# Performance work log

Measured on AMD Instinct MI355X. Metric: run time of the kernel, lower is better.

## Reference

```python
import jax, jax.numpy as jnp
import numpy as np

EPS = 1e-8  # torch F.cosine_similarity eps
TEMP = 2.0  # hardcoded in module regardless of init arg


def _normalize(x):
    # row-normalize with torch-style eps clamp on the norm
    norm = jnp.sqrt(jnp.sum(x * x, axis=-1, keepdims=True))
    return x / jnp.maximum(norm, EPS)


def setup_inputs() -> dict:
    key = jax.random.key(0)
    k1, k2, k3 = jax.random.split(key, 3)
    n, m, d = 8192, 8192, 256
    return {
        "pos_key": jax.random.normal(k1, (n, d), dtype=jnp.float32),
        "pos_value": jax.random.normal(k2, (n, d), dtype=jnp.float32),
        "neg_value": jax.random.normal(k3, (m, d), dtype=jnp.float32),
    }


def reference(pos_key, pos_value, neg_value):
    pk = _normalize(pos_key)    # [n, d]
    pv = _normalize(pos_value)  # [n, d]
    nv = _normalize(neg_value)  # [m, d]

    pos_sim = jnp.sum(pk * pv, axis=-1)          # [n]
    neg_sim = jnp.einsum("nd,md->nm", pk, nv)    # [n, m] cosine sims

    pos_loss = -jnp.mean(pos_sim / TEMP)
    # log-sum-exp over m (stable), matching log(sum(exp(.)))
    neg_loss = jnp.mean(jax.scipy.special.logsumexp(neg_sim / TEMP, axis=-1))
    return pos_loss + neg_loss
```

## Files before the change

### kernel.cpp

```cpp
#include <hip/hip_runtime.h>

typedef __attribute__((ext_vector_type(4))) float f32x4;
typedef __attribute__((ext_vector_type(4))) int   i32x4;
typedef __attribute__((ext_vector_type(8))) int   i32x8;

#define DIM 256
#define D4  64

#define GLD_LDS16(g, l) __builtin_amdgcn_global_load_lds(                      \
    (const __attribute__((address_space(1))) void*)(g),                        \
    (__attribute__((address_space(3))) void*)(l), 16, 0, 0)

__global__ __launch_bounds__(256) void normalize_kernel(
    const float4* __restrict__ pk, const float4* __restrict__ pv,
    const float4* __restrict__ nv, unsigned int* __restrict__ pkn,
    unsigned int* __restrict__ nvn, float* __restrict__ posPart, int N) {
  int row  = blockIdx.x * 4 + (threadIdx.x >> 6);
  int lane = threadIdx.x & 63;
  if (row < N) {
    float4 x = pk[row * D4 + lane];
    float4 y = pv[row * D4 + lane];
    float skk = x.x*x.x + x.y*x.y + x.z*x.z + x.w*x.w;
    float svv = y.x*y.x + y.y*y.y + y.z*y.z + y.w*y.w;
    float skv = x.x*y.x + x.y*y.y + x.z*y.z + x.w*y.w;
#pragma unroll
    for (int m = 32; m >= 1; m >>= 1) {
      skk += __shfl_xor(skk, m, 64);
      svv += __shfl_xor(svv, m, 64);
      skv += __shfl_xor(skv, m, 64);
    }
    float nk  = fmaxf(sqrtf(skk), 1e-8f);
    float nvv = fmaxf(sqrtf(svv), 1e-8f);
    if (lane == 0) posPart[row] = skv / (nk * nvv);
    float rk = 1.0f / nk;
    int w = __builtin_amdgcn_cvt_pk_fp8_f32(x.x * rk, x.y * rk, 0, false);
    w = __builtin_amdgcn_cvt_pk_fp8_f32(x.z * rk, x.w * rk, w, true);
    pkn[(size_t)row * 64 + lane] = (unsigned int)w;
  } else {
    int r2 = row - N;
    float4 x = nv[r2 * D4 + lane];
    float s = x.x*x.x + x.y*x.y + x.z*x.z + x.w*x.w;
#pragma unroll
    for (int m = 32; m >= 1; m >>= 1) s += __shfl_xor(s, m, 64);
    float rn = 1.0f / fmaxf(sqrtf(s), 1e-8f);
    int w = __builtin_amdgcn_cvt_pk_fp8_f32(x.x * rn, x.y * rn, 0, false);
    w = __builtin_amdgcn_cvt_pk_fp8_f32(x.z * rn, x.w * rn, w, true);
    nvn[(size_t)r2 * 64 + lane] = (unsigned int)w;
  }
}

__global__ __launch_bounds__(256, 2) void gemm_lse_kernel(
    const unsigned char* __restrict__ gA, const unsigned char* __restrict__ gB,
    float* __restrict__ partial, int N) {
  __shared__ unsigned char Bs[2][32768];

  const int tid  = threadIdx.x;
  const int lane = tid & 63;
  const int wv   = tid >> 6;
  const int wm   = wv >> 1, wn = wv & 1;
  const int l15  = lane & 15, q = lane >> 4;
  const int row0 = blockIdx.y * 128;
  const int ct0  = blockIdx.x * 8;
  const float kLog2eHalf = 0.72134752044448170f;
  const int kUnitScale = 0x7F7F7F7F;

  const unsigned char* pa = gA + (size_t)(row0 + wm * 64 + l15) * 256 + q * 32;
  i32x4 alo[2][4], ahi[2][4];
#pragma unroll
  for (int kb = 0; kb < 2; kb++)
#pragma unroll
    for (int mi = 0; mi < 4; mi++) {
      alo[kb][mi] = *(const i32x4*)(pa + mi * 4096 + kb * 128);
      ahi[kb][mi] = *(const i32x4*)(pa + mi * 4096 + kb * 128 + 16);
    }

  {
    const unsigned char* pb = gB + (size_t)(ct0 * 128) * 256;
#pragma unroll
    for (int i = 0; i < 8; i++) {
      int c  = i * 256 + tid;
      int r  = c >> 4;
      int sc = ((c & 15) ^ (r & 15)) << 4;
      GLD_LDS16(pb + (size_t)r * 256 + sc, &Bs[0][c * 16]);
    }
  }
  __syncthreads();

  for (int ct = 0; ct < 8; ct++) {
    if (ct < 7) {
      const unsigned char* pb = gB + (size_t)((ct0 + ct + 1) * 128) * 256;
      unsigned char* dst = Bs[(ct + 1) & 1];
#pragma unroll
      for (int i = 0; i < 8; i++) {
        int c  = i * 256 + tid;
        int r  = c >> 4;
        int sc = ((c & 15) ^ (r & 15)) << 4;
        GLD_LDS16(pb + (size_t)r * 256 + sc, dst + c * 16);
      }
    }

    const unsigned char* bs = Bs[ct & 1];
    f32x4 acc[4][4];
#pragma unroll
    for (int mi = 0; mi < 4; mi++)
#pragma unroll
      for (int ni = 0; ni < 4; ni++) acc[mi][ni] = (f32x4){0.f, 0.f, 0.f, 0.f};

#pragma unroll
    for (int kb = 0; kb < 2; kb++) {
      i32x8 bf[4];
#pragma unroll
      for (int ni = 0; ni < 4; ni++) {
        int r  = wn * 64 + ni * 16 + l15;
        int c0 = (kb * 8 + q * 2)     ^ (r & 15);
        int c1 = (kb * 8 + q * 2 + 1) ^ (r & 15);
        i32x4 lo = *(const i32x4*)(bs + r * 256 + c0 * 16);
        i32x4 hi = *(const i32x4*)(bs + r * 256 + c1 * 16);
        bf[ni] = (i32x8){lo.x, lo.y, lo.z, lo.w, hi.x, hi.y, hi.z, hi.w};
      }
#pragma unroll
      for (int mi = 0; mi < 4; mi++) {
        i32x8 af = (i32x8){alo[kb][mi].x, alo[kb][mi].y, alo[kb][mi].z, alo[kb][mi].w,
                           ahi[kb][mi].x, ahi[kb][mi].y, ahi[kb][mi].z, ahi[kb][mi].w};
#pragma unroll
        for (int ni = 0; ni < 4; ni++)
          acc[mi][ni] = __builtin_amdgcn_mfma_scale_f32_16x16x128_f8f6f4(
              af, bf[ni], acc[mi][ni],
              0, 0,
              0, kUnitScale, 0, kUnitScale);
      }
    }

    float keep = 0.f;
#pragma unroll
    for (int mi = 0; mi < 4; mi++)
#pragma unroll
      for (int rr = 0; rr < 4; rr++) {
        float v = 0.f;
#pragma unroll
        for (int ni = 0; ni < 4; ni++)
          v += __builtin_amdgcn_exp2f(acc[mi][ni][rr] * kLog2eHalf);
        v += __shfl_xor(v, 1, 16);
        v += __shfl_xor(v, 2, 16);
        v += __shfl_xor(v, 4, 16);
        v += __shfl_xor(v, 8, 16);
        if (l15 == mi * 4 + rr) keep = v;
      }
    int lrow = (l15 >> 2) * 16 + q * 4 + (l15 & 3);
    partial[(size_t)((ct0 + ct) * 2 + wn) * N + row0 + wm * 64 + lrow] = keep;

    __syncthreads();
  }
}

__global__ __launch_bounds__(256) void finalize_kernel(
    const float* __restrict__ partial, const float* __restrict__ posPart,
    float* __restrict__ out, int N, int slabsPerGroup, float invN) {
  __shared__ float red[4][64];
  int t  = threadIdx.x;
  int rl = t & 63, g = t >> 6;
  int row = blockIdx.x * 64 + rl;
  const float* p = partial + (size_t)(g * slabsPerGroup) * N + row;
  float s = 0.f;
#pragma unroll 8
  for (int j = 0; j < slabsPerGroup; j++) s += p[(size_t)j * N];
  red[g][rl] = s;
  __syncthreads();
  if (t < 64) {
    float tot = red[0][rl] + red[1][rl] + red[2][rl] + red[3][rl];
    float v = __builtin_amdgcn_logf(tot) * 0.69314718055994531f
              - 0.5f * posPart[row];
#pragma unroll
    for (int m = 32; m >= 1; m >>= 1) v += __shfl_xor(v, m, 64);
    if (rl == 0) atomicAdd(out, v * invN);
  }
}

extern "C" void kernel_launch(void* const* d_in, const int* in_sizes, int n_in,
                              void* d_out, int out_size, void* d_ws, size_t ws_size,
                              hipStream_t stream) {
  const float* pk = (const float*)d_in[0];
  const float* pv = (const float*)d_in[1];
  const float* nv = (const float*)d_in[2];
  int N = in_sizes[0] / DIM;
  int M = in_sizes[2] / DIM;
  float* out = (float*)d_out;

  unsigned char* pkn = (unsigned char*)d_ws;
  unsigned char* nvn = pkn + (size_t)N * DIM;
  float* partial = (float*)(nvn + (size_t)M * DIM);
  float* posPart = partial + (size_t)(M / 64) * N;

  hipMemsetAsync(out, 0, sizeof(float), stream);

  normalize_kernel<<<(N + M) / 4, 256, 0, stream>>>(
      (const float4*)pk, (const float4*)pv, (const float4*)nv,
      (unsigned int*)pkn, (unsigned int*)nvn, posPart, N);

  gemm_lse_kernel<<<dim3(M / (128 * 8), N / 128), 256, 0, stream>>>(
      pkn, nvn, partial, N);

  finalize_kernel<<<N / 64, 256, 0, stream>>>(
      partial, posPart, out, N, (M / 64) / 4, 1.0f / (float)N);
}
```

Baseline: 110.3 us.

## Load B fragments straight to registers and accumulate exp sums across tiles

The GEMM kernel no longer stages B tiles through shared memory with barriers. Each wave now loads its B fragments directly from global memory into double-buffered registers. Exp sums are kept in registers across all 8 column tiles, so each wave writes one partial per row per block instead of one per tile. The log2(e)/2 scale is folded into the fp8 normalization (sqrt of the constant applied to both operands), which removes a multiply per exp. In exchange, the two row-waves now fetch the same B data redundantly, and the partial-slab count (16) is hardcoded for the M=8192 shape.

```diff
diff --git a/kernel.cpp b/kernel.cpp
--- a/kernel.cpp
+++ b/kernel.cpp
@@ -7,9 +7,7 @@
 #define DIM 256
 #define D4  64
 
-#define GLD_LDS16(g, l) __builtin_amdgcn_global_load_lds(                      \
-    (const __attribute__((address_space(1))) void*)(g),                        \
-    (__attribute__((address_space(3))) void*)(l), 16, 0, 0)
+#define KSQRTC 0.84932216f
 
 __global__ __launch_bounds__(256) void normalize_kernel(
     const float4* __restrict__ pk, const float4* __restrict__ pv,
@@ -32,7 +30,7 @@
     float nk  = fmaxf(sqrtf(skk), 1e-8f);
     float nvv = fmaxf(sqrtf(svv), 1e-8f);
     if (lane == 0) posPart[row] = skv / (nk * nvv);
-    float rk = 1.0f / nk;
+    float rk = KSQRTC / nk;
     int w = __builtin_amdgcn_cvt_pk_fp8_f32(x.x * rk, x.y * rk, 0, false);
     w = __builtin_amdgcn_cvt_pk_fp8_f32(x.z * rk, x.w * rk, w, true);
     pkn[(size_t)row * 64 + lane] = (unsigned int)w;
@@ -42,7 +40,7 @@
     float s = x.x*x.x + x.y*x.y + x.z*x.z + x.w*x.w;
 #pragma unroll
     for (int m = 32; m >= 1; m >>= 1) s += __shfl_xor(s, m, 64);
-    float rn = 1.0f / fmaxf(sqrtf(s), 1e-8f);
+    float rn = KSQRTC / fmaxf(sqrtf(s), 1e-8f);
     int w = __builtin_amdgcn_cvt_pk_fp8_f32(x.x * rn, x.y * rn, 0, false);
     w = __builtin_amdgcn_cvt_pk_fp8_f32(x.z * rn, x.w * rn, w, true);
     nvn[(size_t)r2 * 64 + lane] = (unsigned int)w;
@@ -52,8 +50,6 @@
 __global__ __launch_bounds__(256, 2) void gemm_lse_kernel(
     const unsigned char* __restrict__ gA, const unsigned char* __restrict__ gB,
     float* __restrict__ partial, int N) {
-  __shared__ unsigned char Bs[2][32768];
-
   const int tid  = threadIdx.x;
   const int lane = tid & 63;
   const int wv   = tid >> 6;
@@ -61,7 +57,6 @@
   const int l15  = lane & 15, q = lane >> 4;
   const int row0 = blockIdx.y * 128;
   const int ct0  = blockIdx.x * 8;
-  const float kLog2eHalf = 0.72134752044448170f;
   const int kUnitScale = 0x7F7F7F7F;
 
   const unsigned char* pa = gA + (size_t)(row0 + wm * 64 + l15) * 256 + q * 32;
@@ -74,83 +69,80 @@
       ahi[kb][mi] = *(const i32x4*)(pa + mi * 4096 + kb * 128 + 16);
     }
 
-  {
-    const unsigned char* pb = gB + (size_t)(ct0 * 128) * 256;
+  const unsigned char* pb =
+      gB + (size_t)(ct0 * 128 + wn * 64 + l15) * 256 + q * 32;
+  i32x4 bbuf[2][8];
 #pragma unroll
-    for (int i = 0; i < 8; i++) {
-      int c  = i * 256 + tid;
-      int r  = c >> 4;
-      int sc = ((c & 15) ^ (r & 15)) << 4;
-      GLD_LDS16(pb + (size_t)r * 256 + sc, &Bs[0][c * 16]);
+  for (int ni = 0; ni < 4; ni++) {
+    bbuf[0][2 * ni]     = *(const i32x4*)(pb + ni * 4096);
+    bbuf[0][2 * ni + 1] = *(const i32x4*)(pb + ni * 4096 + 16);
+  }
+
+  f32x4 acc[4][4];
+#pragma unroll
+  for (int mi = 0; mi < 4; mi++)
+#pragma unroll
+    for (int ni = 0; ni < 4; ni++) acc[mi][ni] = (f32x4){0.f, 0.f, 0.f, 0.f};
+
+  float rp[4][4];
+#pragma unroll
+  for (int a = 0; a < 4; a++)
+#pragma unroll
+    for (int b = 0; b < 4; b++) rp[a][b] = 0.f;
+
+#pragma unroll
+  for (int s = 0; s < 16; s++) {
+    const int kb = s & 1;
+    if (s < 15) {
+      const int t2 = (s + 1) >> 1, kb2 = (s + 1) & 1;
+      const unsigned char* p2 = pb + t2 * 32768 + kb2 * 128;
+#pragma unroll
+      for (int ni = 0; ni < 4; ni++) {
+        bbuf[(s + 1) & 1][2 * ni]     = *(const i32x4*)(p2 + ni * 4096);
+        bbuf[(s + 1) & 1][2 * ni + 1] = *(const i32x4*)(p2 + ni * 4096 + 16);
+      }
+    }
+#pragma unroll
+    for (int mi = 0; mi < 4; mi++) {
+      i32x8 af = (i32x8){alo[kb][mi].x, alo[kb][mi].y, alo[kb][mi].z, alo[kb][mi].w,
+                         ahi[kb][mi].x, ahi[kb][mi].y, ahi[kb][mi].z, ahi[kb][mi].w};
+#pragma unroll
+      for (int ni = 0; ni < 4; ni++) {
+        i32x4 lo = bbuf[s & 1][2 * ni], hi = bbuf[s & 1][2 * ni + 1];
+        i32x8 bf = (i32x8){lo.x, lo.y, lo.z, lo.w, hi.x, hi.y, hi.z, hi.w};
+        acc[mi][ni] = __builtin_amdgcn_mfma_scale_f32_16x16x128_f8f6f4(
+            af, bf, acc[mi][ni],
+            0, 0,
+            0, kUnitScale, 0, kUnitScale);
+      }
+    }
+    if (kb == 1) {
+#pragma unroll
+      for (int mi = 0; mi < 4; mi++)
+#pragma unroll
+        for (int ni = 0; ni < 4; ni++) {
+#pragma unroll
+          for (int rr = 0; rr < 4; rr++)
+            rp[mi][rr] += __builtin_amdgcn_exp2f(acc[mi][ni][rr]);
+          acc[mi][ni] = (f32x4){0.f, 0.f, 0.f, 0.f};
+        }
     }
   }
-  __syncthreads();
 
-  for (int ct = 0; ct < 8; ct++) {
-    if (ct < 7) {
-      const unsigned char* pb = gB + (size_t)((ct0 + ct + 1) * 128) * 256;
-      unsigned char* dst = Bs[(ct + 1) & 1];
+  float keep = 0.f;
 #pragma unroll
-      for (int i = 0; i < 8; i++) {
-        int c  = i * 256 + tid;
-        int r  = c >> 4;
-        int sc = ((c & 15) ^ (r & 15)) << 4;
-        GLD_LDS16(pb + (size_t)r * 256 + sc, dst + c * 16);
-      }
+  for (int mi = 0; mi < 4; mi++)
+#pragma unroll
+    for (int rr = 0; rr < 4; rr++) {
+      float v = rp[mi][rr];
+      v += __shfl_xor(v, 1, 16);
+      v += __shfl_xor(v, 2, 16);
+      v += __shfl_xor(v, 4, 16);
+      v += __shfl_xor(v, 8, 16);
+      if (l15 == mi * 4 + rr) keep = v;
     }
-
-    const unsigned char* bs = Bs[ct & 1];
-    f32x4 acc[4][4];
-#pragma unroll
-    for (int mi = 0; mi < 4; mi++)
-#pragma unroll
-      for (int ni = 0; ni < 4; ni++) acc[mi][ni] = (f32x4){0.f, 0.f, 0.f, 0.f};
-
-#pragma unroll
-    for (int kb = 0; kb < 2; kb++) {
-      i32x8 bf[4];
-#pragma unroll
-      for (int ni = 0; ni < 4; ni++) {
-        int r  = wn * 64 + ni * 16 + l15;
-        int c0 = (kb * 8 + q * 2)     ^ (r & 15);
-        int c1 = (kb * 8 + q * 2 + 1) ^ (r & 15);
-        i32x4 lo = *(const i32x4*)(bs + r * 256 + c0 * 16);
-        i32x4 hi = *(const i32x4*)(bs + r * 256 + c1 * 16);
-        bf[ni] = (i32x8){lo.x, lo.y, lo.z, lo.w, hi.x, hi.y, hi.z, hi.w};
-      }
-#pragma unroll
-      for (int mi = 0; mi < 4; mi++) {
-        i32x8 af = (i32x8){alo[kb][mi].x, alo[kb][mi].y, alo[kb][mi].z, alo[kb][mi].w,
-                           ahi[kb][mi].x, ahi[kb][mi].y, ahi[kb][mi].z, ahi[kb][mi].w};
-#pragma unroll
-        for (int ni = 0; ni < 4; ni++)
-          acc[mi][ni] = __builtin_amdgcn_mfma_scale_f32_16x16x128_f8f6f4(
-              af, bf[ni], acc[mi][ni],
-              0, 0,
-              0, kUnitScale, 0, kUnitScale);
-      }
-    }
-
-    float keep = 0.f;
-#pragma unroll
-    for (int mi = 0; mi < 4; mi++)
-#pragma unroll
-      for (int rr = 0; rr < 4; rr++) {
-        float v = 0.f;
-#pragma unroll
-        for (int ni = 0; ni < 4; ni++)
-          v += __builtin_amdgcn_exp2f(acc[mi][ni][rr] * kLog2eHalf);
-        v += __shfl_xor(v, 1, 16);
-        v += __shfl_xor(v, 2, 16);
-        v += __shfl_xor(v, 4, 16);
-        v += __shfl_xor(v, 8, 16);
-        if (l15 == mi * 4 + rr) keep = v;
-      }
-    int lrow = (l15 >> 2) * 16 + q * 4 + (l15 & 3);
-    partial[(size_t)((ct0 + ct) * 2 + wn) * N + row0 + wm * 64 + lrow] = keep;
-
-    __syncthreads();
-  }
+  int lrow = (l15 >> 2) * 16 + q * 4 + (l15 & 3);
+  partial[(size_t)(blockIdx.x * 2 + wn) * N + row0 + wm * 64 + lrow] = keep;
 }
 
 __global__ __launch_bounds__(256) void finalize_kernel(
@@ -162,7 +154,7 @@
   int row = blockIdx.x * 64 + rl;
   const float* p = partial + (size_t)(g * slabsPerGroup) * N + row;
   float s = 0.f;
-#pragma unroll 8
+#pragma unroll 4
   for (int j = 0; j < slabsPerGroup; j++) s += p[(size_t)j * N];
   red[g][rl] = s;
   __syncthreads();
@@ -189,7 +181,7 @@
   unsigned char* pkn = (unsigned char*)d_ws;
   unsigned char* nvn = pkn + (size_t)N * DIM;
   float* partial = (float*)(nvn + (size_t)M * DIM);
-  float* posPart = partial + (size_t)(M / 64) * N;
+  float* posPart = partial + (size_t)16 * N;
 
   hipMemsetAsync(out, 0, sizeof(float), stream);
 
@@ -201,5 +193,5 @@
       pkn, nvn, partial, N);
 
   finalize_kernel<<<N / 64, 256, 0, stream>>>(
-      partial, posPart, out, N, (M / 64) / 4, 1.0f / (float)N);
+      partial, posPart, out, N, 4, 1.0f / (float)N);
 }
```

New measurement: 155.9 us. +41.4%, slower.
